# Optimization experiments

Measured on AMD Instinct MI355X. Metric: run time of the kernel, lower is better.

Reference implementation:

```python
import jax, jax.numpy as jnp
import numpy as np

NUM_EMBEDDINGS = 8192
EMBEDDING_DIM = 64
COMMITMENT_COST = 0.25


def setup_inputs() -> dict:
    key = jax.random.key(0)
    kx, ke = jax.random.split(key)
    x = jax.random.normal(kx, (32, 1024, EMBEDDING_DIM), dtype=jnp.float32)
    embeddings = jax.random.normal(ke, (NUM_EMBEDDINGS, EMBEDDING_DIM), dtype=jnp.float32)
    return {"x": x, "embeddings": embeddings}


def reference(x, embeddings):
    d = embeddings.shape[1]
    flat_x = x.reshape(-1, d)  # [N, D]
    # squared euclidean distances (argmin identical to cdist argmin):
    d2 = (
        jnp.sum(flat_x * flat_x, axis=-1, keepdims=True)
        - 2.0 * flat_x @ embeddings.T
        + jnp.sum(embeddings * embeddings, axis=-1)
    )
    encoding_indices = jnp.argmin(d2, axis=1)  # [N]
    quantized = embeddings[encoding_indices].reshape(x.shape)
    codebook_loss = jnp.mean((jax.lax.stop_gradient(quantized) - x) ** 2)
    commitment_loss = COMMITMENT_COST * jnp.mean((quantized - jax.lax.stop_gradient(x)) ** 2)
    loss = codebook_loss + commitment_loss
    # straight-through estimator
    quantized_st = x + jax.lax.stop_gradient(quantized - x)
    return quantized_st, loss, encoding_indices
```

## Files before the change

### kernel.cpp

```cpp
#include <hip/hip_runtime.h>
#include <hip/hip_bf16.h>
#include <float.h>

#define N_ROWS 32768
#define DIMS   64
#define K_EMB  8192
#define NT     (K_EMB / 16)
#define NQ     8
#define NTQ    (NT / NQ)
#define RG     4
#define KEYMASK 0xFFFFFFC0u
#define GAP_THR 3.5e-3f

typedef __attribute__((ext_vector_type(8))) short s8v;
typedef __attribute__((ext_vector_type(4))) float f4v;
typedef __attribute__((ext_vector_type(4))) int   i4v;

#define WS_EFRAG 0
#define WS_EN2   (2 * 1024 * 1024)
#define WS_IDX   (WS_EN2 + K_EMB * 4)
#define WS_KEY   (WS_IDX + N_ROWS * 4)
#define WS_BH    (WS_KEY + N_ROWS * 8)
#define WS_SH    (WS_BH + NQ * N_ROWS * 4)
#define WS_CH    (WS_SH + NQ * N_ROWS * 4)
#define WS_NBV   (WS_CH + NQ * N_ROWS * 4)
#define WS_CTL   (WS_NBV + N_ROWS * 4)
#define WS_WL    (WS_CTL + 16)
#define OUT_LOSS (N_ROWS * DIMS)
#define OUT_IDX  (N_ROWS * DIMS + 1)

__device__ inline short bfh(float v) {
    __hip_bfloat16 h = __float2bfloat16(v);
    return __builtin_bit_cast(short, h);
}
__device__ inline float bff(short s) {
    __hip_bfloat16 h = __builtin_bit_cast(__hip_bfloat16, s);
    return __bfloat162float(h);
}

__global__ void vq_prep(const float* __restrict__ emb, short* __restrict__ efrag,
                        float* __restrict__ en2, int4* __restrict__ ctl) {
    if (blockIdx.x == 0 && threadIdx.x == 0) *ctl = make_int4(0, 0, 0, 0);
    int gid = blockIdx.x * 128 + threadIdx.x;
    int t = gid >> 6, lane = gid & 63;
    int m = lane & 15, q = lane >> 4;
    const float* er = emb + (size_t)(t * 16 + m) * DIMS;
    s8v hi0, lo0, hi1, lo1;
    float ss = 0.f;
#pragma unroll
    for (int j = 0; j < 8; ++j) {
        float v0 = er[q * 8 + j];
        float v1 = er[32 + q * 8 + j];
        ss += v0 * v0 + v1 * v1;
        short h0 = bfh(v0); lo0[j] = bfh(v0 - bff(h0)); hi0[j] = h0;
        short h1 = bfh(v1); lo1[j] = bfh(v1 - bff(h1)); hi1[j] = h1;
    }
    s8v* base = (s8v*)efrag + (size_t)t * 4 * 64;
    base[0 * 64 + lane] = hi0;
    base[1 * 64 + lane] = hi1;
    base[2 * 64 + lane] = lo0;
    base[3 * 64 + lane] = lo1;
    ss += __shfl_xor(ss, 16, 64);
    ss += __shfl_xor(ss, 32, 64);
    if (q == 0) en2[t * 16 + m] = -0.5f * ss;
}

#define LOADT(B0, B1, B2, B3, CC, T) do {                 \
    const i4v* _p = bsrc + (size_t)(T) * 256;             \
    B0 = _p[lane];       B1 = _p[64 + lane];              \
    B2 = _p[128 + lane]; B3 = _p[192 + lane];             \
    CC = ep[(T) * 16];                                    \
} while (0)

#define MF(AF, BB, CI) __builtin_amdgcn_mfma_f32_16x16x32_bf16(AF, __builtin_bit_cast(s8v, BB), CI, 0, 0, 0)

#define COMPT(B0, B1, B2, B3, CC, CODE) do {                                     \
    f4v cinit = {CC, CC, CC, CC};                 \
    f4v zf = {0.f, 0.f, 0.f, 0.f};                                               \
    _Pragma("unroll")                                                            \
    for (int g = 0; g < RG; ++g) {                                               \
        f4v pa, pb;                                                              \
        pa = MF(ahi[g][0], B0, cinit);                     \
        pb = MF(ahi[g][1], B1, zf);           \
        pa = MF(ahi[g][0], B2, pa);                                              \
        pb = MF(ahi[g][1], B3, pb);                                              \
        pa = MF(alo[g][0], B0, pa);                                              \
        pb = MF(alo[g][1], B1, pb);                                              \
        f4v acc = pa + pb;                                     \
        _Pragma("unroll")                                                        \
        for (int r = 0; r < 4; ++r) {        \
            float kf = __uint_as_float(                                          \
                (__float_as_uint(acc[r]) & KEYMASK) | (unsigned)(CODE));         \
            sec[g][r]  = __builtin_amdgcn_fmed3f(kf, sec[g][r], best[g][r]);     \
            best[g][r] = fmaxf(best[g][r], kf);                                  \
        }                                                                        \
    }                                                                            \
} while (0)

__global__ __launch_bounds__(64)
__attribute__((amdgpu_waves_per_eu(2, 3))) void vq_phase1(
    const float* __restrict__ x, const short* __restrict__ efrag,
    const float* __restrict__ en2,
    float* __restrict__ bh, float* __restrict__ sh, int* __restrict__ ch) {
    int lane = threadIdx.x;
    int m = lane & 15, q = lane >> 4;
    int kh = blockIdx.y;
    int row0 = blockIdx.x * 64;

    s8v ahi[RG][2], alo[RG][2];
#pragma unroll
    for (int g = 0; g < RG; ++g) {
        const float* xr = x + (size_t)(row0 + g * 16 + m) * DIMS + q * 8;
#pragma unroll
        for (int j = 0; j < 8; ++j) {
            float v0 = xr[j], v1 = xr[32 + j];
            short h0 = bfh(v0); alo[g][0][j] = bfh(v0 - bff(h0)); ahi[g][0][j] = h0;
            short h1 = bfh(v1); alo[g][1][j] = bfh(v1 - bff(h1)); ahi[g][1][j] = h1;
        }
    }

    float best[RG][4], sec[RG][4];
#pragma unroll
    for (int g = 0; g < RG; ++g)
#pragma unroll
        for (int r = 0; r < 4; ++r) { best[g][r] = -FLT_MAX; sec[g][r] = -FLT_MAX; }

    const i4v*   bsrc = (const i4v*)efrag + (size_t)kh * NTQ * 256;
    const float* ep   = en2 + (size_t)kh * NTQ * 16 + m;

    i4v A0, A1, A2, A3, B0, B1, B2, B3;
    float cA, cB;
    LOADT(A0, A1, A2, A3, cA, 0);
#pragma unroll 1
    for (int t = 0; t < NTQ; t += 2) {
        LOADT(B0, B1, B2, B3, cB, t + 1);
        COMPT(A0, A1, A2, A3, cA, t);
        if (t + 2 < NTQ) LOADT(A0, A1, A2, A3, cA, t + 2);
        COMPT(B0, B1, B2, B3, cB, t + 1);
    }

#pragma unroll
    for (int g = 0; g < RG; ++g)
#pragma unroll
    for (int r = 0; r < 4; ++r) {
        float b = best[g][r], sv = sec[g][r];
#pragma unroll
        for (int off = 1; off < 16; off <<= 1) {
            float ob = __shfl_xor(b, off, 64);
            float os = __shfl_xor(sv, off, 64);
            sv = fmaxf(fminf(b, ob), fmaxf(sv, os));
            b  = fmaxf(b, ob);
        }
        unsigned long long bal =
            __ballot(__float_as_uint(best[g][r]) == __float_as_uint(b));
        int win = __ffsll(bal >> (q * 16)) - 1;
        if (m == win) {
            int tl  = (int)(__float_as_uint(b) & 63u);
            int col = ((kh * NTQ + tl) << 4) | m;
            int o = kh * N_ROWS + row0 + g * 16 + q * 4 + r;
            bh[o] = b; sh[o] = sv; ch[o] = col;
        }
    }
}

__global__ void vq_merge(const float* __restrict__ bh, const float* __restrict__ sh,
                         const int* __restrict__ ch, int* __restrict__ idx_buf,
                         unsigned long long* __restrict__ key8,
                         float* __restrict__ nbv,
                         int* __restrict__ wl, int* __restrict__ wl_count) {
    int row = blockIdx.x * 256 + threadIdx.x;
    float nb = bh[row];
    int   c  = ch[row];
    float ns = -FLT_MAX;
#pragma unroll
    for (int h = 1; h < NQ; ++h) {
        float b = bh[h * N_ROWS + row];
        int   cc = ch[h * N_ROWS + row];
        if (b > nb) { ns = nb; nb = b; c = cc; }
        else        { ns = fmaxf(ns, b); }
    }
#pragma unroll
    for (int h = 0; h < NQ; ++h) ns = fmaxf(ns, sh[h * N_ROWS + row]);
    idx_buf[row] = c;
    key8[row] = 0ULL;
    nbv[row] = nb;
    if (nb - ns < GAP_THR) {
        int pos = atomicAdd(wl_count, 1);
        wl[pos] = row;
    }
}

__global__ __launch_bounds__(64) void vq_fixup(
    const float* __restrict__ x, const float* __restrict__ emb,
    const float* __restrict__ en2, const float* __restrict__ nbv,
    unsigned long long* __restrict__ key8,
    const int* __restrict__ wl, const int* __restrict__ wl_count) {
    int lane = threadIdx.x;
    int cchunk = blockIdx.x & 127;
    int rslice = blockIdx.x >> 7;
    int cnt = *wl_count;
    if (rslice >= cnt) return;
    int c = cchunk * 64 + lane;
    const float4* er = (const float4*)(emb + (size_t)c * DIMS);
    float4 e[16];
#pragma unroll
    for (int qq = 0; qq < 16; ++qq) e[qq] = er[qq];
    float c0 = en2[c];
    for (int wi = rslice; wi < cnt; wi += 16) {
        int row = wl[wi];
        const float4* xr = (const float4*)(x + (size_t)row * DIMS);
        float d = 0.f;
#pragma unroll
        for (int qq = 0; qq < 16; ++qq) {
            float4 ee = e[qq];
            float4 xx = xr[qq];
            d += ee.x * xx.x + ee.y * xx.y + ee.z * xx.z + ee.w * xx.w;
        }
        float bf_ = d + c0;
        int bc_ = c;
#pragma unroll
        for (int off = 1; off < 64; off <<= 1) {
            float of = __shfl_xor(bf_, off, 64);
            int   oc = __shfl_xor(bc_, off, 64);
            if (of > bf_ || (of == bf_ && oc < bc_)) { bf_ = of; bc_ = oc; }
        }
        if (lane == 0 && bf_ >= nbv[row] - GAP_THR) {
            unsigned int u = __float_as_uint(bf_);
            unsigned int sb = ((int)u < 0) ? ~u : (u | 0x80000000u);
            unsigned long long key = ((unsigned long long)sb << 32) | (unsigned int)(~bc_);
            atomicMax(&key8[row], key);
        }
    }
}

__global__ void vq_gather(const float* __restrict__ x, const float* __restrict__ emb,
                          const int* __restrict__ idx_buf,
                          const unsigned long long* __restrict__ key8,
                          float* __restrict__ out, double* __restrict__ loss_acc,
                          int* __restrict__ done_count) {
    int row = blockIdx.x * blockDim.x + threadIdx.x;
    unsigned long long k = key8[row];
    int idx = k ? (int)(~(unsigned int)k) : idx_buf[row];
    const float4* ev = (const float4*)(emb + (size_t)idx * DIMS);
    const float4* xv = (const float4*)(x + (size_t)row * DIMS);
    float4* ov = (float4*)(out + (size_t)row * DIMS);
    float s = 0.f;
#pragma unroll
    for (int qq = 0; qq < 16; ++qq) {
        float4 ee = ev[qq];
        float4 xx = xv[qq];
        float dx = ee.x - xx.x, dy = ee.y - xx.y, dz = ee.z - xx.z, dw = ee.w - xx.w;
        s += dx * dx + dy * dy + dz * dz + dw * dw;
        ov[qq] = ee;
    }
#pragma unroll
    for (int off = 32; off > 0; off >>= 1) s += __shfl_down(s, off, 64);
    if ((threadIdx.x & 63) == 0) atomicAdd(loss_acc, (double)s);
    out[OUT_IDX + row] = (float)idx;
    __syncthreads();
    if (threadIdx.x == 0) {
        __threadfence();
        int d = atomicAdd(done_count, 1);
        if (d == (int)gridDim.x - 1) {
            double total = atomicAdd(loss_acc, 0.0);
            out[OUT_LOSS] = (float)(1.25 * total / (double)(N_ROWS * DIMS));
        }
    }
}

extern "C" void kernel_launch(void* const* d_in, const int* in_sizes, int n_in,
                              void* d_out, int out_size, void* d_ws, size_t ws_size,
                              hipStream_t stream) {
    const float* x   = (const float*)d_in[0];
    const float* emb = (const float*)d_in[1];
    float* out = (float*)d_out;
    char*  ws  = (char*)d_ws;

    short* efrag   = (short*)(ws + WS_EFRAG);
    float* en2     = (float*)(ws + WS_EN2);
    int*   idx_buf = (int*)(ws + WS_IDX);
    unsigned long long* key8 = (unsigned long long*)(ws + WS_KEY);
    float* bhb     = (float*)(ws + WS_BH);
    float* shb     = (float*)(ws + WS_SH);
    int*   chb     = (int*)(ws + WS_CH);
    float* nbv     = (float*)(ws + WS_NBV);
    double* loss_acc = (double*)(ws + WS_CTL);
    int*   wl_count  = (int*)(ws + WS_CTL + 8);
    int*   done_cnt  = (int*)(ws + WS_CTL + 12);
    int*   wl        = (int*)(ws + WS_WL);

    vq_prep<<<(NT * 64) / 128, 128, 0, stream>>>(emb, efrag, en2, (int4*)(ws + WS_CTL));
    vq_phase1<<<dim3(N_ROWS / 64, NQ), 64, 0, stream>>>(x, efrag, en2, bhb, shb, chb);
    vq_merge<<<N_ROWS / 256, 256, 0, stream>>>(bhb, shb, chb, idx_buf, key8, nbv, wl, wl_count);
    vq_fixup<<<2048, 64, 0, stream>>>(x, emb, en2, nbv, key8, wl, wl_count);
    vq_gather<<<N_ROWS / 256, 256, 0, stream>>>(x, emb, idx_buf, key8, out, loss_acc, done_cnt);
}
```

Measured before the change: 200.4 us.

## Replace split-bf16 triple MFMA with single fp16 MFMA and widen fixup margin

The distance GEMM drops the hi/lo bf16 split, which needed three MFMA passes per K-half, and uses one fp16 MFMA per K-half instead. This halves the codebook fragment memory and cuts matrix work about threefold. The lower precision is covered by raising the near-tie gap threshold so more rows go to the exact fp32 fixup pass. The fixup grid is doubled to absorb the larger worklist, and the occupancy hint is relaxed. The trade is that fixup work grows with the worklist, and fp16 overflow or rounding may miss true argmins if the margin is too small.

```diff
diff --git a/kernel.cpp b/kernel.cpp
--- a/kernel.cpp
+++ b/kernel.cpp
@@ -1,5 +1,6 @@
 #include <hip/hip_runtime.h>
 #include <hip/hip_bf16.h>
+#include <hip/hip_fp16.h>
 #include <float.h>
 
 #define N_ROWS 32768
@@ -10,11 +11,12 @@
 #define NTQ    (NT / NQ)
 #define RG     4
 #define KEYMASK 0xFFFFFFC0u
-#define GAP_THR 3.5e-3f
-
-typedef __attribute__((ext_vector_type(8))) short s8v;
-typedef __attribute__((ext_vector_type(4))) float f4v;
-typedef __attribute__((ext_vector_type(4))) int   i4v;
+#define GAP_THR 0.06f
+
+typedef __attribute__((ext_vector_type(8))) short    s8v;
+typedef __attribute__((ext_vector_type(8))) _Float16 h8v;
+typedef __attribute__((ext_vector_type(4))) float    f4v;
+typedef __attribute__((ext_vector_type(4))) int      i4v;
 
 #define WS_EFRAG 0
 #define WS_EN2   (2 * 1024 * 1024)
@@ -29,13 +31,9 @@
 #define OUT_LOSS (N_ROWS * DIMS)
 #define OUT_IDX  (N_ROWS * DIMS + 1)
 
-__device__ inline short bfh(float v) {
-    __hip_bfloat16 h = __float2bfloat16(v);
+__device__ inline short hfh(float v) {
+    _Float16 h = (_Float16)v;
     return __builtin_bit_cast(short, h);
-}
-__device__ inline float bff(short s) {
-    __hip_bfloat16 h = __builtin_bit_cast(__hip_bfloat16, s);
-    return __bfloat162float(h);
 }
 
 __global__ void vq_prep(const float* __restrict__ emb, short* __restrict__ efrag,
@@ -45,48 +43,39 @@
     int t = gid >> 6, lane = gid & 63;
     int m = lane & 15, q = lane >> 4;
     const float* er = emb + (size_t)(t * 16 + m) * DIMS;
-    s8v hi0, lo0, hi1, lo1;
+    s8v f0, f1;
     float ss = 0.f;
 #pragma unroll
     for (int j = 0; j < 8; ++j) {
         float v0 = er[q * 8 + j];
         float v1 = er[32 + q * 8 + j];
         ss += v0 * v0 + v1 * v1;
-        short h0 = bfh(v0); lo0[j] = bfh(v0 - bff(h0)); hi0[j] = h0;
-        short h1 = bfh(v1); lo1[j] = bfh(v1 - bff(h1)); hi1[j] = h1;
-    }
-    s8v* base = (s8v*)efrag + (size_t)t * 4 * 64;
-    base[0 * 64 + lane] = hi0;
-    base[1 * 64 + lane] = hi1;
-    base[2 * 64 + lane] = lo0;
-    base[3 * 64 + lane] = lo1;
+        f0[j] = hfh(v0);
+        f1[j] = hfh(v1);
+    }
+    s8v* base = (s8v*)efrag + (size_t)t * 2 * 64;
+    base[0 * 64 + lane] = f0;
+    base[1 * 64 + lane] = f1;
     ss += __shfl_xor(ss, 16, 64);
     ss += __shfl_xor(ss, 32, 64);
     if (q == 0) en2[t * 16 + m] = -0.5f * ss;
 }
 
-#define LOADT(B0, B1, B2, B3, CC, T) do {                 \
-    const i4v* _p = bsrc + (size_t)(T) * 256;             \
-    B0 = _p[lane];       B1 = _p[64 + lane];              \
-    B2 = _p[128 + lane]; B3 = _p[192 + lane];             \
+#define LOADT(P0, P1, CC, T) do {                         \
+    const i4v* _p = bsrc + (size_t)(T) * 128;             \
+    P0 = _p[lane];  P1 = _p[64 + lane];                   \
     CC = ep[(T) * 16];                                    \
 } while (0)
 
-#define MF(AF, BB, CI) __builtin_amdgcn_mfma_f32_16x16x32_bf16(AF, __builtin_bit_cast(s8v, BB), CI, 0, 0, 0)
-
-#define COMPT(B0, B1, B2, B3, CC, CODE) do {                                     \
+#define MF16(AF, BB, CI) __builtin_amdgcn_mfma_f32_16x16x32_f16(AF, __builtin_bit_cast(h8v, BB), CI, 0, 0, 0)
+
+#define COMPT(P0, P1, CC, CODE) do {                                             \
     f4v cinit = {CC, CC, CC, CC};                 \
-    f4v zf = {0.f, 0.f, 0.f, 0.f};                                               \
     _Pragma("unroll")                                                            \
     for (int g = 0; g < RG; ++g) {                                               \
-        f4v pa, pb;                                                              \
-        pa = MF(ahi[g][0], B0, cinit);                     \
-        pb = MF(ahi[g][1], B1, zf);           \
-        pa = MF(ahi[g][0], B2, pa);                                              \
-        pb = MF(ahi[g][1], B3, pb);                                              \
-        pa = MF(alo[g][0], B0, pa);                                              \
-        pb = MF(alo[g][1], B1, pb);                                              \
-        f4v acc = pa + pb;                                     \
+        f4v acc;                                                                 \
+        acc = MF16(ah[g][0], P0, cinit);                                         \
+        acc = MF16(ah[g][1], P1, acc);                                           \
         _Pragma("unroll")                                                        \
         for (int r = 0; r < 4; ++r) {        \
             float kf = __uint_as_float(                                          \
@@ -98,7 +87,7 @@
 } while (0)
 
 __global__ __launch_bounds__(64)
-__attribute__((amdgpu_waves_per_eu(2, 3))) void vq_phase1(
+__attribute__((amdgpu_waves_per_eu(2, 4))) void vq_phase1(
     const float* __restrict__ x, const short* __restrict__ efrag,
     const float* __restrict__ en2,
     float* __restrict__ bh, float* __restrict__ sh, int* __restrict__ ch) {
@@ -107,15 +96,14 @@
     int kh = blockIdx.y;
     int row0 = blockIdx.x * 64;
 
-    s8v ahi[RG][2], alo[RG][2];
+    h8v ah[RG][2];
 #pragma unroll
     for (int g = 0; g < RG; ++g) {
         const float* xr = x + (size_t)(row0 + g * 16 + m) * DIMS + q * 8;
 #pragma unroll
         for (int j = 0; j < 8; ++j) {
-            float v0 = xr[j], v1 = xr[32 + j];
-            short h0 = bfh(v0); alo[g][0][j] = bfh(v0 - bff(h0)); ahi[g][0][j] = h0;
-            short h1 = bfh(v1); alo[g][1][j] = bfh(v1 - bff(h1)); ahi[g][1][j] = h1;
+            ah[g][0][j] = (_Float16)xr[j];
+            ah[g][1][j] = (_Float16)xr[32 + j];
         }
     }
 
@@ -125,18 +113,18 @@
 #pragma unroll
         for (int r = 0; r < 4; ++r) { best[g][r] = -FLT_MAX; sec[g][r] = -FLT_MAX; }
 
-    const i4v*   bsrc = (const i4v*)efrag + (size_t)kh * NTQ * 256;
+    const i4v*   bsrc = (const i4v*)efrag + (size_t)kh * NTQ * 128;
     const float* ep   = en2 + (size_t)kh * NTQ * 16 + m;
 
-    i4v A0, A1, A2, A3, B0, B1, B2, B3;
+    i4v A0, A1, B0, B1;
     float cA, cB;
-    LOADT(A0, A1, A2, A3, cA, 0);
+    LOADT(A0, A1, cA, 0);
 #pragma unroll 1
     for (int t = 0; t < NTQ; t += 2) {
-        LOADT(B0, B1, B2, B3, cB, t + 1);
-        COMPT(A0, A1, A2, A3, cA, t);
-        if (t + 2 < NTQ) LOADT(A0, A1, A2, A3, cA, t + 2);
-        COMPT(B0, B1, B2, B3, cB, t + 1);
+        LOADT(B0, B1, cB, t + 1);
+        COMPT(A0, A1, cA, t);
+        if (t + 2 < NTQ) LOADT(A0, A1, cA, t + 2);
+        COMPT(B0, B1, cB, t + 1);
     }
 
 #pragma unroll
@@ -206,7 +194,7 @@
 #pragma unroll
     for (int qq = 0; qq < 16; ++qq) e[qq] = er[qq];
     float c0 = en2[c];
-    for (int wi = rslice; wi < cnt; wi += 16) {
+    for (int wi = rslice; wi < cnt; wi += 32) {
         int row = wl[wi];
         const float4* xr = (const float4*)(x + (size_t)row * DIMS);
         float d = 0.f;
@@ -292,6 +280,6 @@
     vq_prep<<<(NT * 64) / 128, 128, 0, stream>>>(emb, efrag, en2, (int4*)(ws + WS_CTL));
     vq_phase1<<<dim3(N_ROWS / 64, NQ), 64, 0, stream>>>(x, efrag, en2, bhb, shb, chb);
     vq_merge<<<N_ROWS / 256, 256, 0, stream>>>(bhb, shb, chb, idx_buf, key8, nbv, wl, wl_count);
-    vq_fixup<<<2048, 64, 0, stream>>>(x, emb, en2, nbv, key8, wl, wl_count);
+    vq_fixup<<<4096, 64, 0, stream>>>(x, emb, en2, nbv, key8, wl, wl_count);
     vq_gather<<<N_ROWS / 256, 256, 0, stream>>>(x, emb, idx_buf, key8, out, loss_acc, done_cnt);
 }
```

Result: slower. 222.6 us (+11.1%).
